# Kernel optimization log

Hardware: AMD Instinct MI355X
Metric: run time of the kernel (lower is better)

## Reference

```python
import jax, jax.numpy as jnp
import numpy as np

B, N, TF, DM = 16, 4096, 512, 1024

def next_fast_len(n):
    # smallest 5-smooth number >= n (matches scipy.fftpack.next_fast_len)
    while True:
        m = n
        for p in (2, 3, 5):
            while m % p == 0:
                m //= p
        if m == 1:
            return n
        n += 1

def conv1d_fft(x, weights):
    # x: (..., N, F), weights: (M,); causal exponentially-weighted correlation
    n = x.shape[-2]
    m = weights.shape[-1]
    L = next_fast_len(n + m - 1)
    f_x = jnp.fft.rfft(x, n=L, axis=-2)                 # (..., Lr, F) complex
    f_w = jnp.fft.rfft(weights, n=L, axis=-1)           # (Lr,)
    out = jnp.fft.irfft(f_x * jnp.conj(f_w)[..., None], L, axis=-2)
    out = jnp.roll(out, -1, axis=-2)
    return out[..., L - n:, :]                           # last N along seq axis

def setup_inputs() -> dict:
    key = jax.random.key(0)
    ks = jax.random.split(key, 8)
    inp = {
        "x": jax.random.normal(ks[0], (B, N, TF), dtype=jnp.float32),
        "latent_growth": jax.random.normal(ks[1], (B, N, DM), dtype=jnp.float32),
        "latent_seasonal": jax.random.normal(ks[2], (B, N, DM), dtype=jnp.float32),
        "alpha": jnp.zeros((1,), dtype=jnp.float32),  # nn.Parameter(torch.Tensor([0.0]))
        "w_growth": jax.random.normal(ks[3], (TF, DM), dtype=jnp.float32) / np.sqrt(DM),
        "b_growth": jnp.zeros((TF,), dtype=jnp.float32),
        "w_seasonal": jax.random.normal(ks[4], (TF, DM), dtype=jnp.float32) / np.sqrt(DM),
        "b_seasonal": jnp.zeros((TF,), dtype=jnp.float32),
    }
    return inp

def reference(x, latent_growth, latent_seasonal, alpha, w_growth, b_growth, w_seasonal, b_seasonal):
    n = x.shape[1]
    a = jax.nn.sigmoid(alpha)[0]
    powers = jnp.arange(n, dtype=x.dtype)[::-1]          # flipped arange
    seasonal = jnp.einsum('bnd,fd->bnf', latent_seasonal, w_seasonal) + b_seasonal
    aes_weights = a * (1.0 - a) ** powers                # alpha*(1-alpha)^k EMA kernel
    seasonal_normalized_term = conv1d_fft(x - seasonal, aes_weights)
    # NOTE: the original module computes `growth` but does not use it in the output
    growth = jnp.einsum('bnd,fd->bnf', latent_growth, w_growth) + b_growth
    growth_term = conv1d_fft(x, aes_weights)
    return seasonal_normalized_term + growth_term
```

## Files before the change

### kernel.cpp

```cpp
#include <hip/hip_runtime.h>
#include <math.h>

#define B_DIM 16
#define N_SEQ 4096
#define TF_DIM 512
#define DM_DIM 1024
#define CHUNK 128
#define NCHUNK (N_SEQ / CHUNK)
#define NKT (DM_DIM / 32)

typedef __attribute__((ext_vector_type(4))) float f32x4;
typedef __attribute__((ext_vector_type(8))) short bf16x8;

__device__ __forceinline__ unsigned short f2bf(float f) {
    unsigned int u = __builtin_bit_cast(unsigned int, f);
    u += 0x7fffu + ((u >> 16) & 1u);
    return (unsigned short)(u >> 16);
}

__global__ __launch_bounds__(256, 2)
void gemm_u_kernel(const float* __restrict__ x,
                   const float* __restrict__ ls,
                   const float* __restrict__ wmat,
                   const float* __restrict__ bias,
                   const float* __restrict__ alpha,
                   float* __restrict__ u,
                   float* __restrict__ e)
{
    __shared__ unsigned short As[2][4096];
    __shared__ unsigned short Ws[2][4096];
    __shared__ float red[2][4][16];

    const int tid  = threadIdx.x;
    const int f0   = blockIdx.x * 128;
    const int row0 = blockIdx.y * 128;

    const int lane = tid & 63;
    const int wid  = tid >> 6;
    const int wm = wid >> 1, wn = wid & 1;
    const int l15 = lane & 15, l4 = lane >> 4;

    const int srow = tid >> 2;
    const int ke   = (tid & 3) * 8;
    const int sxor = (srow & 7) << 3;
    const int sidx1 = (srow * 32 + ke) ^ sxor;
    const int sidx2 = ((srow + 64) * 32 + ke) ^ sxor;

    const float* aptr1 = ls   + (size_t)(row0 + srow) * DM_DIM + ke;
    const float* aptr2 = aptr1 + (size_t)64 * DM_DIM;
    const float* wptr1 = wmat + (size_t)(f0 + srow) * DM_DIM + ke;
    const float* wptr2 = wptr1 + (size_t)64 * DM_DIM;

    int rofa[4], rofw[4];
    const int rxor = (l15 & 7) << 3;
#pragma unroll
    for (int i = 0; i < 4; ++i) {
        rofa[i] = ((wm * 64 + i * 16 + l15) * 32 + l4 * 8) ^ rxor;
        rofw[i] = ((wn * 64 + i * 16 + l15) * 32 + l4 * 8) ^ rxor;
    }

    f32x4 acc[4][4];
#pragma unroll
    for (int i = 0; i < 4; ++i)
#pragma unroll
        for (int j = 0; j < 4; ++j) acc[i][j] = (f32x4){0.f, 0.f, 0.f, 0.f};

    f32x4 A00, A01, A02, A03, W00, W01, W02, W03;
    f32x4 A10, A11, A12, A13, W10, W11, W12, W13;

#define LOAD_SET(SA, SW, KT) do {                                        \
        const int _ko = (KT) * 32;                                       \
        SA##0 = *(const f32x4*)(aptr1 + _ko);                            \
        SA##1 = *(const f32x4*)(aptr1 + _ko + 4);                        \
        SA##2 = *(const f32x4*)(aptr2 + _ko);                            \
        SA##3 = *(const f32x4*)(aptr2 + _ko + 4);                        \
        SW##0 = *(const f32x4*)(wptr1 + _ko);                            \
        SW##1 = *(const f32x4*)(wptr1 + _ko + 4);                        \
        SW##2 = *(const f32x4*)(wptr2 + _ko);                            \
        SW##3 = *(const f32x4*)(wptr2 + _ko + 4);                        \
    } while (0)

#define PACK8(V0, V1) ({                                                  \
        union { unsigned short s[8]; bf16x8 v; } _p;                     \
        _p.s[0] = f2bf(V0[0]); _p.s[1] = f2bf(V0[1]);                    \
        _p.s[2] = f2bf(V0[2]); _p.s[3] = f2bf(V0[3]);                    \
        _p.s[4] = f2bf(V1[0]); _p.s[5] = f2bf(V1[1]);                    \
        _p.s[6] = f2bf(V1[2]); _p.s[7] = f2bf(V1[3]);                    \
        _p.v; })

#define WRITE_SET(BUF, SA, SW) do {                                      \
        *(bf16x8*)(&As[BUF][sidx1]) = PACK8(SA##0, SA##1);               \
        *(bf16x8*)(&As[BUF][sidx2]) = PACK8(SA##2, SA##3);               \
        *(bf16x8*)(&Ws[BUF][sidx1]) = PACK8(SW##0, SW##1);               \
        *(bf16x8*)(&Ws[BUF][sidx2]) = PACK8(SW##2, SW##3);               \
    } while (0)

#define COMPUTE(BUF) do {                                                \
        const unsigned short* _Ab = As[BUF];                             \
        const unsigned short* _Wb = Ws[BUF];                             \
        bf16x8 _af[4], _wf[4];                                           \
        _Pragma("unroll")                                                \
        for (int i = 0; i < 4; ++i) {                                    \
            _af[i] = *(const bf16x8*)(_Ab + rofa[i]);                    \
            _wf[i] = *(const bf16x8*)(_Wb + rofw[i]);                    \
        }                                                                \
        _Pragma("unroll")                                                \
        for (int mi = 0; mi < 4; ++mi)                                   \
        _Pragma("unroll")                                                \
        for (int ni = 0; ni < 4; ++ni)                                   \
            acc[mi][ni] = __builtin_amdgcn_mfma_f32_16x16x32_bf16(       \
                _af[mi], _wf[ni], acc[mi][ni], 0, 0, 0);                 \
    } while (0)

    LOAD_SET(A0, W0, 0);
    LOAD_SET(A1, W1, 1);
    WRITE_SET(0, A0, W0);
    __syncthreads();

#pragma unroll 1
    for (int kt = 0; kt < NKT; kt += 2) {
        if (kt + 2 < NKT) LOAD_SET(A0, W0, kt + 2);
        COMPUTE(0);
        WRITE_SET(1, A1, W1);
        __syncthreads();
        if (kt + 3 < NKT) LOAD_SET(A1, W1, kt + 3);
        COMPUTE(1);
        if (kt + 2 < NKT) WRITE_SET(0, A0, W0);
        __syncthreads();
    }

    const float a = 1.0f / (1.0f + expf(-alpha[0]));
    const float c = 1.0f - a;
    const float l2c = log2f(c);

    float bia[4];
#pragma unroll
    for (int ni = 0; ni < 4; ++ni) bia[ni] = bias[f0 + wn * 64 + ni * 16 + l15];

    float epart[4] = {0.f, 0.f, 0.f, 0.f};

#pragma unroll
    for (int mi = 0; mi < 4; ++mi) {
#pragma unroll
        for (int j = 0; j < 4; ++j) {
            const int r = wm * 64 + mi * 16 + l4 * 4 + j;
            const size_t rb = (size_t)(row0 + r) * TF_DIM;
            const float wgt = (r == CHUNK - 1)
                                  ? a
                                  : a * exp2f((float)(CHUNK - 1 - r) * l2c);
#pragma unroll
            for (int ni = 0; ni < 4; ++ni) {
                const int f = f0 + wn * 64 + ni * 16 + l15;
                const float uval = 2.0f * x[rb + f] - (acc[mi][ni][j] + bia[ni]);
                u[rb + f] = uval;
                epart[ni] = fmaf(wgt, uval, epart[ni]);
            }
        }
    }

#pragma unroll
    for (int ni = 0; ni < 4; ++ni) {
        epart[ni] += __shfl_xor(epart[ni], 16, 64);
        epart[ni] += __shfl_xor(epart[ni], 32, 64);
    }
    if (wm == 1 && l4 == 0) {
#pragma unroll
        for (int ni = 0; ni < 4; ++ni) red[wn][ni][l15] = epart[ni];
    }
    __syncthreads();
    if (wm == 0 && l4 == 0) {
#pragma unroll
        for (int ni = 0; ni < 4; ++ni) {
            const int f = f0 + wn * 64 + ni * 16 + l15;
            e[(size_t)blockIdx.y * TF_DIM + f] = epart[ni] + red[wn][ni][l15];
        }
    }
}

__global__ __launch_bounds__(256)
void ema_carry(const float* __restrict__ e, const float* __restrict__ alpha,
               float* __restrict__ carry)
{
    const int idx = blockIdx.x * 256 + threadIdx.x;
    const int f = idx & (TF_DIM - 1);
    const int b = idx >> 9;
    const float a = 1.0f / (1.0f + expf(-alpha[0]));
    const float c = 1.0f - a;
    const float cC = exp2f((float)CHUNK * log2f(c));
    const size_t base = (size_t)b * NCHUNK * TF_DIM + f;
    float Y = 0.0f;
    carry[base] = 0.0f;
    for (int ch = 1; ch < NCHUNK; ++ch) {
        Y = fmaf(cC, Y, e[base + (size_t)(ch - 1) * TF_DIM]);
        carry[base + (size_t)ch * TF_DIM] = Y;
    }
}

__global__ __launch_bounds__(256)
void ema_apply(const float* __restrict__ u, const float* __restrict__ carry,
               const float* __restrict__ alpha, float* __restrict__ out)
{
    const int idx = blockIdx.x * 256 + threadIdx.x;
    const int f = idx & (TF_DIM - 1);
    const int bc = idx >> 9;
    const float a = 1.0f / (1.0f + expf(-alpha[0]));
    const float c = 1.0f - a;
    float y = carry[idx];
    const float* up = u + (size_t)bc * CHUNK * TF_DIM + f;
    float* op = out + (size_t)bc * CHUNK * TF_DIM + f;
#pragma unroll 4
    for (int j = 0; j < CHUNK; ++j) {
        y = fmaf(c, y, a * up[(size_t)j * TF_DIM]);
        op[(size_t)j * TF_DIM] = y;
    }
}

extern "C" void kernel_launch(void* const* d_in, const int* in_sizes, int n_in,
                              void* d_out, int out_size, void* d_ws, size_t ws_size,
                              hipStream_t stream) {
    const float* x     = (const float*)d_in[0];
    const float* ls    = (const float*)d_in[2];
    const float* alpha = (const float*)d_in[3];
    const float* wmat  = (const float*)d_in[6];
    const float* bias  = (const float*)d_in[7];
    float* out = (float*)d_out;

    float* u     = (float*)d_ws;
    float* e     = u + (size_t)B_DIM * N_SEQ * TF_DIM;
    float* carry = e + (size_t)B_DIM * NCHUNK * TF_DIM;

    dim3 g1(TF_DIM / 128, B_DIM * N_SEQ / 128);
    gemm_u_kernel<<<g1, 256, 0, stream>>>(x, ls, wmat, bias, alpha, u, e);

    const int tot = B_DIM * NCHUNK * TF_DIM;
    ema_carry<<<(B_DIM * TF_DIM) / 256, 256, 0, stream>>>(e, alpha, carry);
    ema_apply<<<tot / 256, 256, 0, stream>>>(u, carry, alpha, out);
}
```

Baseline: 267.5 us.

## Stage GEMM tiles via direct global-to-LDS loads and store intermediate in bf16

The GEMM now copies fp32 tiles straight from global memory into LDS with global_load_lds, which removes the register staging and the per-element software bf16 rounding. Conversion to bf16 moves to fragment-read time using the hardware packed convert instruction, and the LDS footprint doubles to fp32 tiles. The intermediate u buffer is written as bf16 instead of fp32, which halves its write and read traffic. The EMA apply kernel is reorganized to process two features per thread with vectorized loads and stores. Storing u in bf16 adds rounding error to the output, and the larger LDS use may reduce occupancy.

```diff
diff --git a/kernel.cpp b/kernel.cpp
--- a/kernel.cpp
+++ b/kernel.cpp
@@ -11,11 +11,35 @@
 
 typedef __attribute__((ext_vector_type(4))) float f32x4;
 typedef __attribute__((ext_vector_type(8))) short bf16x8;
-
-__device__ __forceinline__ unsigned short f2bf(float f) {
-    unsigned int u = __builtin_bit_cast(unsigned int, f);
+typedef unsigned short u16;
+typedef unsigned int u32;
+
+__device__ __forceinline__ u16 f2bf(float f) {
+    u32 u = __builtin_bit_cast(u32, f);
     u += 0x7fffu + ((u >> 16) & 1u);
-    return (unsigned short)(u >> 16);
+    return (u16)(u >> 16);
+}
+
+__device__ __forceinline__ void gload16(const float* g, float* l) {
+    __builtin_amdgcn_global_load_lds(
+        (const __attribute__((address_space(1))) void*)g,
+        (__attribute__((address_space(3))) void*)l,
+        16, 0, 0);
+}
+
+__device__ __forceinline__ u32 cvtpk(float lo, float hi) {
+    u32 r;
+    asm("v_cvt_pk_bf16_f32 %0, %1, %2" : "=v"(r) : "v"(lo), "v"(hi));
+    return r;
+}
+
+__device__ __forceinline__ bf16x8 pack8(f32x4 v0, f32x4 v1) {
+    union { u32 u[4]; bf16x8 v; } p;
+    p.u[0] = cvtpk(v0[0], v0[1]);
+    p.u[1] = cvtpk(v0[2], v0[3]);
+    p.u[2] = cvtpk(v1[0], v1[1]);
+    p.u[3] = cvtpk(v1[2], v1[3]);
+    return p.v;
 }
 
 __global__ __launch_bounds__(256, 2)
@@ -24,11 +48,11 @@
                    const float* __restrict__ wmat,
                    const float* __restrict__ bias,
                    const float* __restrict__ alpha,
-                   float* __restrict__ u,
+                   u16* __restrict__ u,
                    float* __restrict__ e)
 {
-    __shared__ unsigned short As[2][4096];
-    __shared__ unsigned short Ws[2][4096];
+    __shared__ float As[2][4096];
+    __shared__ float Ws[2][4096];
     __shared__ float red[2][4][16];
 
     const int tid  = threadIdx.x;
@@ -40,24 +64,27 @@
     const int wm = wid >> 1, wn = wid & 1;
     const int l15 = lane & 15, l4 = lane >> 4;
 
-    const int srow = tid >> 2;
-    const int ke   = (tid & 3) * 8;
-    const int sxor = (srow & 7) << 3;
-    const int sidx1 = (srow * 32 + ke) ^ sxor;
-    const int sidx2 = ((srow + 64) * 32 + ke) ^ sxor;
-
-    const float* aptr1 = ls   + (size_t)(row0 + srow) * DM_DIM + ke;
-    const float* aptr2 = aptr1 + (size_t)64 * DM_DIM;
-    const float* wptr1 = wmat + (size_t)(f0 + srow) * DM_DIM + ke;
-    const float* wptr2 = wptr1 + (size_t)64 * DM_DIM;
-
-    int rofa[4], rofw[4];
-    const int rxor = (l15 & 7) << 3;
-#pragma unroll
-    for (int i = 0; i < 4; ++i) {
-        rofa[i] = ((wm * 64 + i * 16 + l15) * 32 + l4 * 8) ^ rxor;
-        rofw[i] = ((wn * 64 + i * 16 + l15) * 32 + l4 * 8) ^ rxor;
-    }
+    const int sr = wid * 32 + (lane >> 3);
+    const int sc = ((lane & 7) ^ ((lane >> 3) & 7)) * 4;
+    const float* aSrc = ls   + (size_t)(row0 + sr) * DM_DIM + sc;
+    const float* wSrc = wmat + (size_t)(f0   + sr) * DM_DIM + sc;
+    const int ldsb = wid * 1024;
+
+#define STAGE(BUF, KT) do {                                              \
+        const int _ko = (KT) * 32;                                       \
+        gload16(aSrc + _ko,         &As[BUF][ldsb]);                     \
+        gload16(aSrc + _ko +  8192, &As[BUF][ldsb + 256]);               \
+        gload16(aSrc + _ko + 16384, &As[BUF][ldsb + 512]);               \
+        gload16(aSrc + _ko + 24576, &As[BUF][ldsb + 768]);               \
+        gload16(wSrc + _ko,         &Ws[BUF][ldsb]);                     \
+        gload16(wSrc + _ko +  8192, &Ws[BUF][ldsb + 256]);               \
+        gload16(wSrc + _ko + 16384, &Ws[BUF][ldsb + 512]);               \
+        gload16(wSrc + _ko + 24576, &Ws[BUF][ldsb + 768]);               \
+    } while (0)
+
+    const int xr   = (l15 & 7) << 2;
+    const int aoff = (wm * 64 + l15) * 32 + ((l4 * 8) ^ xr);
+    const int woff = (wn * 64 + l15) * 32 + ((l4 * 8) ^ xr);
 
     f32x4 acc[4][4];
 #pragma unroll
@@ -65,44 +92,21 @@
 #pragma unroll
         for (int j = 0; j < 4; ++j) acc[i][j] = (f32x4){0.f, 0.f, 0.f, 0.f};
 
-    f32x4 A00, A01, A02, A03, W00, W01, W02, W03;
-    f32x4 A10, A11, A12, A13, W10, W11, W12, W13;
-
-#define LOAD_SET(SA, SW, KT) do {                                        \
-        const int _ko = (KT) * 32;                                       \
-        SA##0 = *(const f32x4*)(aptr1 + _ko);                            \
-        SA##1 = *(const f32x4*)(aptr1 + _ko + 4);                        \
-        SA##2 = *(const f32x4*)(aptr2 + _ko);                            \
-        SA##3 = *(const f32x4*)(aptr2 + _ko + 4);                        \
-        SW##0 = *(const f32x4*)(wptr1 + _ko);                            \
-        SW##1 = *(const f32x4*)(wptr1 + _ko + 4);                        \
-        SW##2 = *(const f32x4*)(wptr2 + _ko);                            \
-        SW##3 = *(const f32x4*)(wptr2 + _ko + 4);                        \
-    } while (0)
-
-#define PACK8(V0, V1) ({                                                  \
-        union { unsigned short s[8]; bf16x8 v; } _p;                     \
-        _p.s[0] = f2bf(V0[0]); _p.s[1] = f2bf(V0[1]);                    \
-        _p.s[2] = f2bf(V0[2]); _p.s[3] = f2bf(V0[3]);                    \
-        _p.s[4] = f2bf(V1[0]); _p.s[5] = f2bf(V1[1]);                    \
-        _p.s[6] = f2bf(V1[2]); _p.s[7] = f2bf(V1[3]);                    \
-        _p.v; })
-
-#define WRITE_SET(BUF, SA, SW) do {                                      \
-        *(bf16x8*)(&As[BUF][sidx1]) = PACK8(SA##0, SA##1);               \
-        *(bf16x8*)(&As[BUF][sidx2]) = PACK8(SA##2, SA##3);               \
-        *(bf16x8*)(&Ws[BUF][sidx1]) = PACK8(SW##0, SW##1);               \
-        *(bf16x8*)(&Ws[BUF][sidx2]) = PACK8(SW##2, SW##3);               \
-    } while (0)
-
 #define COMPUTE(BUF) do {                                                \
-        const unsigned short* _Ab = As[BUF];                             \
-        const unsigned short* _Wb = Ws[BUF];                             \
+        const float* _Ab = &As[BUF][0];                                  \
+        const float* _Wb = &Ws[BUF][0];                                  \
         bf16x8 _af[4], _wf[4];                                           \
         _Pragma("unroll")                                                \
         for (int i = 0; i < 4; ++i) {                                    \
-            _af[i] = *(const bf16x8*)(_Ab + rofa[i]);                    \
-            _wf[i] = *(const bf16x8*)(_Wb + rofw[i]);                    \
+            f32x4 _v0 = *(const f32x4*)(_Ab + (aoff + i * 512));         \
+            f32x4 _v1 = *(const f32x4*)(_Ab + ((aoff ^ 4) + i * 512));   \
+            _af[i] = pack8(_v0, _v1);                                    \
+        }                                                                \
+        _Pragma("unroll")                                                \
+        for (int i = 0; i < 4; ++i) {                                    \
+            f32x4 _v0 = *(const f32x4*)(_Wb + (woff + i * 512));         \
+            f32x4 _v1 = *(const f32x4*)(_Wb + ((woff ^ 4) + i * 512));   \
+            _wf[i] = pack8(_v0, _v1);                                    \
         }                                                                \
         _Pragma("unroll")                                                \
         for (int mi = 0; mi < 4; ++mi)                                   \
@@ -112,20 +116,16 @@
                 _af[mi], _wf[ni], acc[mi][ni], 0, 0, 0);                 \
     } while (0)
 
-    LOAD_SET(A0, W0, 0);
-    LOAD_SET(A1, W1, 1);
-    WRITE_SET(0, A0, W0);
+    STAGE(0, 0);
     __syncthreads();
 
 #pragma unroll 1
     for (int kt = 0; kt < NKT; kt += 2) {
-        if (kt + 2 < NKT) LOAD_SET(A0, W0, kt + 2);
+        if (kt + 1 < NKT) STAGE(1, kt + 1);
         COMPUTE(0);
-        WRITE_SET(1, A1, W1);
         __syncthreads();
-        if (kt + 3 < NKT) LOAD_SET(A1, W1, kt + 3);
+        if (kt + 2 < NKT) STAGE(0, kt + 2);
         COMPUTE(1);
-        if (kt + 2 < NKT) WRITE_SET(0, A0, W0);
         __syncthreads();
     }
 
@@ -152,7 +152,7 @@
             for (int ni = 0; ni < 4; ++ni) {
                 const int f = f0 + wn * 64 + ni * 16 + l15;
                 const float uval = 2.0f * x[rb + f] - (acc[mi][ni][j] + bia[ni]);
-                u[rb + f] = uval;
+                u[rb + f] = f2bf(uval);
                 epart[ni] = fmaf(wgt, uval, epart[ni]);
             }
         }
@@ -197,21 +197,25 @@
 }
 
 __global__ __launch_bounds__(256)
-void ema_apply(const float* __restrict__ u, const float* __restrict__ carry,
+void ema_apply(const u16* __restrict__ u, const float* __restrict__ carry,
                const float* __restrict__ alpha, float* __restrict__ out)
 {
-    const int idx = blockIdx.x * 256 + threadIdx.x;
-    const int f = idx & (TF_DIM - 1);
-    const int bc = idx >> 9;
+    const int bc = blockIdx.x;
+    const int tid = threadIdx.x;
     const float a = 1.0f / (1.0f + expf(-alpha[0]));
     const float c = 1.0f - a;
-    float y = carry[idx];
-    const float* up = u + (size_t)bc * CHUNK * TF_DIM + f;
-    float* op = out + (size_t)bc * CHUNK * TF_DIM + f;
+    float y0 = carry[(size_t)bc * TF_DIM + 2 * tid];
+    float y1 = carry[(size_t)bc * TF_DIM + 2 * tid + 1];
+    const u32* up = (const u32*)(u + (size_t)bc * CHUNK * TF_DIM) + tid;
+    float2*    op = (float2*)(out + (size_t)bc * CHUNK * TF_DIM) + tid;
 #pragma unroll 4
     for (int j = 0; j < CHUNK; ++j) {
-        y = fmaf(c, y, a * up[(size_t)j * TF_DIM]);
-        op[(size_t)j * TF_DIM] = y;
+        const u32 w = up[(size_t)j * (TF_DIM / 2)];
+        const float u0 = __builtin_bit_cast(float, (w & 0xffffu) << 16);
+        const float u1 = __builtin_bit_cast(float, (w >> 16) << 16);
+        y0 = fmaf(c, y0, a * u0);
+        y1 = fmaf(c, y1, a * u1);
+        op[(size_t)j * (TF_DIM / 2)] = make_float2(y0, y1);
     }
 }
 
@@ -225,14 +229,13 @@
     const float* bias  = (const float*)d_in[7];
     float* out = (float*)d_out;
 
-    float* u     = (float*)d_ws;
-    float* e     = u + (size_t)B_DIM * N_SEQ * TF_DIM;
+    u16*   u     = (u16*)d_ws;
+    float* e     = (float*)(u + (size_t)B_DIM * N_SEQ * TF_DIM);
     float* carry = e + (size_t)B_DIM * NCHUNK * TF_DIM;
 
     dim3 g1(TF_DIM / 128, B_DIM * N_SEQ / 128);
     gemm_u_kernel<<<g1, 256, 0, stream>>>(x, ls, wmat, bias, alpha, u, e);
 
-    const int tot = B_DIM * NCHUNK * TF_DIM;
     ema_carry<<<(B_DIM * TF_DIM) / 256, 256, 0, stream>>>(e, alpha, carry);
-    ema_apply<<<tot / 256, 256, 0, stream>>>(u, carry, alpha, out);
-}
+    ema_apply<<<B_DIM * NCHUNK, 256, 0, stream>>>(u, carry, alpha, out);
+}
```

Result: slower. 279.0 us (+4.3%).

## Store intermediate u as bf16, use packed bf16 convert, lighter barriers

Applied to the files above, without the earlier changes.

Stores the intermediate u buffer as bf16 instead of fp32, halving the write traffic in the GEMM epilogue and the read traffic in ema_apply. ema_apply is reorganised so each thread handles two adjacent features, with a 32-bit load and a float2 store. The bf16 packing for the GEMM operands now uses the v_cvt_pk_bf16_f32 instruction instead of manual rounding, and __syncthreads is replaced with an lgkmcnt wait plus s_barrier. Launch bounds are raised to 4 blocks per SM. Rounding u to bf16 adds error to the EMA inputs, while the chunk carries are still computed from the fp32 values.

```diff
diff --git a/kernel.cpp b/kernel.cpp
--- a/kernel.cpp
+++ b/kernel.cpp
@@ -11,20 +11,30 @@
 
 typedef __attribute__((ext_vector_type(4))) float f32x4;
 typedef __attribute__((ext_vector_type(8))) short bf16x8;
-
-__device__ __forceinline__ unsigned short f2bf(float f) {
-    unsigned int u = __builtin_bit_cast(unsigned int, f);
+typedef unsigned short u16;
+typedef unsigned int u32;
+
+__device__ __forceinline__ u16 f2bf(float f) {
+    u32 u = __builtin_bit_cast(u32, f);
     u += 0x7fffu + ((u >> 16) & 1u);
-    return (unsigned short)(u >> 16);
-}
-
-__global__ __launch_bounds__(256, 2)
+    return (u16)(u >> 16);
+}
+
+__device__ __forceinline__ u32 cvtpk(float lo, float hi) {
+    u32 r;
+    asm("v_cvt_pk_bf16_f32 %0, %1, %2" : "=v"(r) : "v"(lo), "v"(hi));
+    return r;
+}
+
+#define BARRIER_PUB() asm volatile("s_waitcnt lgkmcnt(0)\n\ts_barrier" ::: "memory")
+
+__global__ __launch_bounds__(256, 4)
 void gemm_u_kernel(const float* __restrict__ x,
                    const float* __restrict__ ls,
                    const float* __restrict__ wmat,
                    const float* __restrict__ bias,
                    const float* __restrict__ alpha,
-                   float* __restrict__ u,
+                   u16* __restrict__ u,
                    float* __restrict__ e)
 {
     __shared__ unsigned short As[2][4096];
@@ -81,11 +91,11 @@
     } while (0)
 
 #define PACK8(V0, V1) ({                                                  \
-        union { unsigned short s[8]; bf16x8 v; } _p;                     \
-        _p.s[0] = f2bf(V0[0]); _p.s[1] = f2bf(V0[1]);                    \
-        _p.s[2] = f2bf(V0[2]); _p.s[3] = f2bf(V0[3]);                    \
-        _p.s[4] = f2bf(V1[0]); _p.s[5] = f2bf(V1[1]);                    \
-        _p.s[6] = f2bf(V1[2]); _p.s[7] = f2bf(V1[3]);                    \
+        union { u32 u[4]; bf16x8 v; } _p;                                \
+        _p.u[0] = cvtpk(V0[0], V0[1]);                                   \
+        _p.u[1] = cvtpk(V0[2], V0[3]);                                   \
+        _p.u[2] = cvtpk(V1[0], V1[1]);                                   \
+        _p.u[3] = cvtpk(V1[2], V1[3]);                                   \
         _p.v; })
 
 #define WRITE_SET(BUF, SA, SW) do {                                      \
@@ -115,18 +125,19 @@
     LOAD_SET(A0, W0, 0);
     LOAD_SET(A1, W1, 1);
     WRITE_SET(0, A0, W0);
-    __syncthreads();
+    BARRIER_PUB();
 
 #pragma unroll 1
     for (int kt = 0; kt < NKT; kt += 2) {
         if (kt + 2 < NKT) LOAD_SET(A0, W0, kt + 2);
         COMPUTE(0);
         WRITE_SET(1, A1, W1);
-        __syncthreads();
+        BARRIER_PUB();
+
         if (kt + 3 < NKT) LOAD_SET(A1, W1, kt + 3);
         COMPUTE(1);
         if (kt + 2 < NKT) WRITE_SET(0, A0, W0);
-        __syncthreads();
+        BARRIER_PUB();
     }
 
     const float a = 1.0f / (1.0f + expf(-alpha[0]));
@@ -152,7 +163,7 @@
             for (int ni = 0; ni < 4; ++ni) {
                 const int f = f0 + wn * 64 + ni * 16 + l15;
                 const float uval = 2.0f * x[rb + f] - (acc[mi][ni][j] + bia[ni]);
-                u[rb + f] = uval;
+                u[rb + f] = f2bf(uval);
                 epart[ni] = fmaf(wgt, uval, epart[ni]);
             }
         }
@@ -197,21 +208,25 @@
 }
 
 __global__ __launch_bounds__(256)
-void ema_apply(const float* __restrict__ u, const float* __restrict__ carry,
+void ema_apply(const u16* __restrict__ u, const float* __restrict__ carry,
                const float* __restrict__ alpha, float* __restrict__ out)
 {
-    const int idx = blockIdx.x * 256 + threadIdx.x;
-    const int f = idx & (TF_DIM - 1);
-    const int bc = idx >> 9;
+    const int bc = blockIdx.x;
+    const int tid = threadIdx.x;
     const float a = 1.0f / (1.0f + expf(-alpha[0]));
     const float c = 1.0f - a;
-    float y = carry[idx];
-    const float* up = u + (size_t)bc * CHUNK * TF_DIM + f;
-    float* op = out + (size_t)bc * CHUNK * TF_DIM + f;
+    float y0 = carry[(size_t)bc * TF_DIM + 2 * tid];
+    float y1 = carry[(size_t)bc * TF_DIM + 2 * tid + 1];
+    const u32* up = (const u32*)(u + (size_t)bc * CHUNK * TF_DIM) + tid;
+    float2*    op = (float2*)(out + (size_t)bc * CHUNK * TF_DIM) + tid;
 #pragma unroll 4
     for (int j = 0; j < CHUNK; ++j) {
-        y = fmaf(c, y, a * up[(size_t)j * TF_DIM]);
-        op[(size_t)j * TF_DIM] = y;
+        const u32 w = up[(size_t)j * (TF_DIM / 2)];
+        const float u0 = __builtin_bit_cast(float, (w & 0xffffu) << 16);
+        const float u1 = __builtin_bit_cast(float, (w >> 16) << 16);
+        y0 = fmaf(c, y0, a * u0);
+        y1 = fmaf(c, y1, a * u1);
+        op[(size_t)j * (TF_DIM / 2)] = make_float2(y0, y1);
     }
 }
 
@@ -225,14 +240,13 @@
     const float* bias  = (const float*)d_in[7];
     float* out = (float*)d_out;
 
-    float* u     = (float*)d_ws;
-    float* e     = u + (size_t)B_DIM * N_SEQ * TF_DIM;
+    u16*   u     = (u16*)d_ws;
+    float* e     = (float*)(u + (size_t)B_DIM * N_SEQ * TF_DIM);
     float* carry = e + (size_t)B_DIM * NCHUNK * TF_DIM;
 
     dim3 g1(TF_DIM / 128, B_DIM * N_SEQ / 128);
     gemm_u_kernel<<<g1, 256, 0, stream>>>(x, ls, wmat, bias, alpha, u, e);
 
-    const int tot = B_DIM * NCHUNK * TF_DIM;
     ema_carry<<<(B_DIM * TF_DIM) / 256, 256, 0, stream>>>(e, alpha, carry);
-    ema_apply<<<tot / 256, 256, 0, stream>>>(u, carry, alpha, out);
-}
+    ema_apply<<<B_DIM * NCHUNK, 256, 0, stream>>>(u, carry, alpha, out);
+}
```

Measured after the change: 811.2 us. 203% more time.
